# Kernel optimization log

Hardware: AMD Instinct MI355X
Metric: run time of the kernel (lower is better)

The kernel has to match this reference:

```python
import jax, jax.numpy as jnp
import numpy as np

B_SZ, L, D_INNER = 2, 1024, 2048
D_STATE, DT_RANK = 16, 64


def setup_inputs() -> dict:
    key = jax.random.key(0)
    k1, k2, k3, k4 = jax.random.split(key, 4)
    x = jax.random.normal(k1, (B_SZ, L, D_INNER), dtype=jnp.float32)
    # Linear weights: torch layout (out_features, in_features); scaled ~1/sqrt(fan_in)
    W_x = jax.random.normal(k2, (DT_RANK + 2 * D_STATE, D_INNER), dtype=jnp.float32) / np.sqrt(D_INNER)
    W_dt = jax.random.normal(k3, (D_INNER, DT_RANK), dtype=jnp.float32) / np.sqrt(DT_RANK)
    b_dt = jax.random.normal(k4, (D_INNER,), dtype=jnp.float32) * 0.1
    # A_log = log(arange(1, d_state+1)) broadcast to (d_inner, d_state), as in __init__
    A_log = jnp.broadcast_to(jnp.log(jnp.arange(1, D_STATE + 1, dtype=jnp.float32)), (D_INNER, D_STATE))
    D = jnp.ones((D_INNER,), dtype=jnp.float32)
    return {"x": x, "W_x": W_x, "W_dt": W_dt, "b_dt": b_dt, "A_log": A_log, "D": D}


def reference(x, W_x, W_dt, b_dt, A_log, D):
    # x: (B, L, d_inner)
    xz = jnp.einsum('bld,kd->blk', x, W_x)                       # (B, L, dt_rank + 2*d_state)
    delta_raw = xz[..., :DT_RANK]
    B_in = xz[..., DT_RANK:DT_RANK + D_STATE]                    # (B, L, d_state)
    C_in = xz[..., DT_RANK + D_STATE:]                           # (B, L, d_state)
    delta = jax.nn.softplus(jnp.einsum('blr,dr->bld', delta_raw, W_dt) + b_dt)  # (B, L, d_inner)
    A = -jnp.exp(A_log)                                          # (d_inner, d_state), negative
    A_bar = jnp.exp(delta[..., None] * A)                        # (B, L, d_inner, d_state)
    B_bar = delta[..., None] * B_in[:, :, None, :]               # (B, L, d_inner, d_state)

    def step(h, inputs):
        A_t, Bx_t, C_t = inputs                                  # (B,d,n), (B,d,n), (B,n)
        h = A_t * h + Bx_t
        y_t = jnp.sum(h * C_t[:, None, :], axis=-1)              # (B, d_inner)
        return h, y_t

    h0 = jnp.zeros((x.shape[0], D_INNER, D_STATE), dtype=x.dtype)
    Bx = B_bar * x[..., None]                                    # (B, L, d_inner, d_state)
    # scan over L: move L to leading axis
    _, ys = jax.lax.scan(step, h0, (jnp.moveaxis(A_bar, 1, 0), jnp.moveaxis(Bx, 1, 0), jnp.moveaxis(C_in, 1, 0)))
    y = jnp.moveaxis(ys, 0, 1) + D * x                           # (B, L, d_inner)
    return y
```

## Files before the change

### kernel.cpp

```cpp
#include <hip/hip_runtime.h>
#include <hip/hip_bf16.h>

#define B_SZ 2
#define LSEQ 1024
#define DIN  2048
#define DST  16
#define DTR  64
#define KTOT 96
#define NROW (B_SZ * LSEQ)
#define NCH  64
#define TCH  16
#define KSP  32

__device__ __forceinline__ float b2f(unsigned int u) {
    union { unsigned int i; float f; } v;
    v.i = (u & 0xffffu) << 16;
    return v.f;
}

__device__ __forceinline__ float ldf(const void* p, size_t i, bool f32) {
    return f32 ? ((const float*)p)[i] : b2f(((const unsigned short*)p)[i]);
}

__device__ __forceinline__ float4 ld4(const void* p, size_t i, bool f32) {
    if (f32) return *(const float4*)((const float*)p + i);
    const uint2 u = *(const uint2*)((const unsigned short*)p + i);
    float4 v;
    v.x = b2f(u.x); v.y = b2f(u.x >> 16);
    v.z = b2f(u.y); v.w = b2f(u.y >> 16);
    return v;
}

__device__ __forceinline__ float softplus_f(float v) {
    return (v > 20.f) ? v : log1pf(__expf(v));
}

__global__ __launch_bounds__(256) void k_detect(const void* __restrict__ x,
                                                int* __restrict__ flag) {
    __shared__ int cnt;
    if (threadIdx.x == 0) cnt = 0;
    __syncthreads();
    const unsigned short* u = (const unsigned short*)x;
    int my = 0;
    for (int i = threadIdx.x; i < 4096; i += 256) {
        unsigned short v = u[2 * i];
        float af = fabsf(b2f(v));
        if (v == 0 || (af >= 6.0e-8f && af <= 1.7e7f)) my++;
    }
    atomicAdd(&cnt, my);
    __syncthreads();
    if (threadIdx.x == 0) *flag = (cnt < 2048) ? 1 : 0;
}

__global__ __launch_bounds__(256, 4) void k_proj(
    const void* __restrict__ x,
    const void* __restrict__ Wx,
    const int*  __restrict__ flag,
    float* __restrict__ part)
{
    const bool f32 = (*flag != 0);
    __shared__ float lx[32][68];
    __shared__ float lw[32][100];
    const int tid = threadIdx.x;
    const int bx = blockIdx.x;
    const int by = blockIdx.y;
    const int rt = tid >> 4, ct = tid & 15;
    const int r0 = rt * 4, c0 = ct * 6;

    float acc[4][6];
    #pragma unroll
    for (int i = 0; i < 4; i++)
        #pragma unroll
        for (int k = 0; k < 6; k++) acc[i][k] = 0.f;

    for (int half = 0; half < 2; half++) {
        const int k0 = by * 64 + half * 32;
        #pragma unroll
        for (int it = 0; it < 2; it++) {
            const int idx = tid + it * 256;
            const int r = idx >> 3, q = idx & 7;
            float4 v = ld4(x, (size_t)(bx * 64 + r) * DIN + k0 + q * 4, f32);
            lx[q * 4 + 0][r] = v.x; lx[q * 4 + 1][r] = v.y;
            lx[q * 4 + 2][r] = v.z; lx[q * 4 + 3][r] = v.w;
        }
        #pragma unroll
        for (int it = 0; it < 3; it++) {
            const int idx = tid + it * 256;
            const int c = idx >> 3, q = idx & 7;
            float4 v = ld4(Wx, (size_t)c * DIN + k0 + q * 4, f32);
            lw[q * 4 + 0][c] = v.x; lw[q * 4 + 1][c] = v.y;
            lw[q * 4 + 2][c] = v.z; lw[q * 4 + 3][c] = v.w;
        }
        __syncthreads();

        #pragma unroll 4
        for (int j = 0; j < 32; j++) {
            const float4 xa = *(const float4*)&lx[j][r0];
            const float2 w0 = *(const float2*)&lw[j][c0];
            const float2 w1 = *(const float2*)&lw[j][c0 + 2];
            const float2 w2 = *(const float2*)&lw[j][c0 + 4];
            const float xr[4] = {xa.x, xa.y, xa.z, xa.w};
            const float wc[6] = {w0.x, w0.y, w1.x, w1.y, w2.x, w2.y};
            #pragma unroll
            for (int i = 0; i < 4; i++)
                #pragma unroll
                for (int k = 0; k < 6; k++)
                    acc[i][k] += xr[i] * wc[k];
        }
        __syncthreads();
    }

    float* p = part + ((size_t)by * NROW + bx * 64 + r0) * KTOT + c0;
    #pragma unroll
    for (int i = 0; i < 4; i++) {
        float* row = p + (size_t)i * KTOT;
        *(float2*)(row)     = make_float2(acc[i][0], acc[i][1]);
        *(float2*)(row + 2) = make_float2(acc[i][2], acc[i][3]);
        *(float2*)(row + 4) = make_float2(acc[i][4], acc[i][5]);
    }
}

__global__ __launch_bounds__(256, 4) void k_comb(
    const float* __restrict__ part,
    float* __restrict__ drw, float* __restrict__ Bin, float* __restrict__ Cin)
{
    const int idx = blockIdx.x * 256 + threadIdx.x;
    float s = 0.f;
    #pragma unroll 8
    for (int ks = 0; ks < KSP; ks++)
        s += part[(size_t)ks * NROW * KTOT + idx];
    const int r = idx / KTOT, c = idx % KTOT;
    if (c < DTR)            drw[r * DTR + c] = s;
    else if (c < DTR + DST) Bin[r * DST + (c - DTR)] = s;
    else                    Cin[r * DST + (c - DTR - DST)] = s;
}

__global__ __launch_bounds__(256, 4) void k_dt(
    const float* __restrict__ drw,
    const void* __restrict__ Wdt,
    const void* __restrict__ bdt,
    const int*  __restrict__ flag,
    float* __restrict__ dt)
{
    const bool f32 = (*flag != 0);
    __shared__ float la[64][68];
    __shared__ float lb[64][68];
    const int tid = threadIdx.x;
    const int r0g = blockIdx.x * 64, c0g = blockIdx.y * 64;

    #pragma unroll
    for (int it = 0; it < 4; it++) {
        const int idx = tid + it * 256;
        const int r = idx >> 4, q = idx & 15;
        float4 v = *(const float4*)(drw + (size_t)(r0g + r) * DTR + q * 4);
        la[q * 4 + 0][r] = v.x; la[q * 4 + 1][r] = v.y;
        la[q * 4 + 2][r] = v.z; la[q * 4 + 3][r] = v.w;
    }
    #pragma unroll
    for (int it = 0; it < 4; it++) {
        const int idx = tid + it * 256;
        const int c = idx >> 4, q = idx & 15;
        float4 v = ld4(Wdt, (size_t)(c0g + c) * DTR + q * 4, f32);
        lb[q * 4 + 0][c] = v.x; lb[q * 4 + 1][c] = v.y;
        lb[q * 4 + 2][c] = v.z; lb[q * 4 + 3][c] = v.w;
    }
    __syncthreads();

    const int rt = tid >> 4, ct = tid & 15;
    const int r0 = rt * 4, c0 = ct * 4;
    float acc[4][4];
    #pragma unroll
    for (int i = 0; i < 4; i++)
        #pragma unroll
        for (int k = 0; k < 4; k++) acc[i][k] = 0.f;

    #pragma unroll 8
    for (int j = 0; j < 64; j++) {
        const float4 a = *(const float4*)&la[j][r0];
        const float4 b = *(const float4*)&lb[j][c0];
        const float ar[4] = {a.x, a.y, a.z, a.w};
        const float bc[4] = {b.x, b.y, b.z, b.w};
        #pragma unroll
        for (int i = 0; i < 4; i++)
            #pragma unroll
            for (int k = 0; k < 4; k++)
                acc[i][k] += ar[i] * bc[k];
    }

    float bd[4];
    #pragma unroll
    for (int k = 0; k < 4; k++) bd[k] = ldf(bdt, (size_t)(c0g + c0 + k), f32);
    #pragma unroll
    for (int i = 0; i < 4; i++) {
        float4 o;
        o.x = softplus_f(acc[i][0] + bd[0]);
        o.y = softplus_f(acc[i][1] + bd[1]);
        o.z = softplus_f(acc[i][2] + bd[2]);
        o.w = softplus_f(acc[i][3] + bd[3]);
        *(float4*)(dt + (size_t)(r0g + r0 + i) * DIN + c0g + c0) = o;
    }
}

__global__ __launch_bounds__(256, 4) void k_scan1(
    const void* __restrict__ x,
    const float* __restrict__ dt,
    const float* __restrict__ Bin,
    const void* __restrict__ Alog,
    const int*  __restrict__ flag,
    float* __restrict__ Pb,
    float* __restrict__ Hb)
{
    const bool f32 = (*flag != 0);
    __shared__ float Bs[TCH * DST];
    const int tid = threadIdx.x;
    const int d = blockIdx.x * 256 + tid;
    const int c = blockIdx.y;
    const int b = blockIdx.z;
    const int row0 = b * LSEQ + c * TCH;

    if (tid < TCH * DST) Bs[tid] = Bin[(size_t)row0 * DST + tid];

    float A[DST];
    #pragma unroll
    for (int sq = 0; sq < DST / 4; sq++) {
        float4 av = ld4(Alog, (size_t)d * DST + sq * 4, f32);
        A[sq * 4 + 0] = -__expf(av.x); A[sq * 4 + 1] = -__expf(av.y);
        A[sq * 4 + 2] = -__expf(av.z); A[sq * 4 + 3] = -__expf(av.w);
    }
    __syncthreads();

    float P[DST], H[DST];
    #pragma unroll
    for (int s = 0; s < DST; s++) { P[s] = 1.f; H[s] = 0.f; }

    #pragma unroll 4
    for (int t = 0; t < TCH; t++) {
        const size_t off = (size_t)(row0 + t) * DIN + d;
        const float dtv = dt[off];
        const float xv  = ldf(x, off, f32);
        const float u   = dtv * xv;
        const float* bs = Bs + t * DST;
        #pragma unroll
        for (int s = 0; s < DST; s++) {
            const float e = __expf(dtv * A[s]);
            P[s] *= e;
            H[s] = e * H[s] + u * bs[s];
        }
    }

    const size_t base = (size_t)(b * NCH + c) * DST * DIN + d;
    #pragma unroll
    for (int s = 0; s < DST; s++) {
        Pb[base + (size_t)s * DIN] = P[s];
        Hb[base + (size_t)s * DIN] = H[s];
    }
}

__global__ __launch_bounds__(256, 4) void k_scan2(
    float* __restrict__ Pb,
    const float* __restrict__ Hb)
{
    const int idx = blockIdx.x * 256 + threadIdx.x;
    const int b   = idx / (DST * DIN);
    const int rem = idx % (DST * DIN);
    float h = 0.f;
    #pragma unroll 4
    for (int c = 0; c < NCH; c++) {
        const size_t o = (size_t)(b * NCH + c) * DST * DIN + rem;
        const float p = Pb[o], hb = Hb[o];
        Pb[o] = h;
        h = hb + p * h;
    }
}

__global__ __launch_bounds__(256, 4) void k_scan3(
    const void* __restrict__ x,
    const float* __restrict__ dt,
    const float* __restrict__ Bin,
    const float* __restrict__ Cin,
    const void* __restrict__ Alog,
    const void* __restrict__ Dv,
    const float* __restrict__ hin,
    const int*  __restrict__ flag,
    void* __restrict__ y)
{
    const bool f32 = (*flag != 0);
    __shared__ float Bs[TCH * DST];
    __shared__ float Cs[TCH * DST];
    const int tid = threadIdx.x;
    const int d = blockIdx.x * 256 + tid;
    const int c = blockIdx.y;
    const int b = blockIdx.z;
    const int row0 = b * LSEQ + c * TCH;

    if (tid < TCH * DST) {
        Bs[tid] = Bin[(size_t)row0 * DST + tid];
        Cs[tid] = Cin[(size_t)row0 * DST + tid];
    }

    float A[DST];
    #pragma unroll
    for (int sq = 0; sq < DST / 4; sq++) {
        float4 av = ld4(Alog, (size_t)d * DST + sq * 4, f32);
        A[sq * 4 + 0] = -__expf(av.x); A[sq * 4 + 1] = -__expf(av.y);
        A[sq * 4 + 2] = -__expf(av.z); A[sq * 4 + 3] = -__expf(av.w);
    }
    const float Dd = ldf(Dv, (size_t)d, f32);
    __syncthreads();

    float h[DST];
    const size_t base = (size_t)(b * NCH + c) * DST * DIN + d;
    #pragma unroll
    for (int s = 0; s < DST; s++) h[s] = hin[base + (size_t)s * DIN];

    #pragma unroll 4
    for (int t = 0; t < TCH; t++) {
        const size_t off = (size_t)(row0 + t) * DIN + d;
        const float dtv = dt[off];
        const float xv  = ldf(x, off, f32);
        const float u   = dtv * xv;
        const float* bs = Bs + t * DST;
        const float* cs = Cs + t * DST;
        float yv = Dd * xv;
        #pragma unroll
        for (int s = 0; s < DST; s++) {
            const float e = __expf(dtv * A[s]);
            h[s] = e * h[s] + u * bs[s];
            yv += h[s] * cs[s];
        }
        if (f32) ((float*)y)[off] = yv;
        else     ((__hip_bfloat16*)y)[off] = __float2bfloat16(yv);
    }
}

extern "C" void kernel_launch(void* const* d_in, const int* in_sizes, int n_in,
                              void* d_out, int out_size, void* d_ws, size_t ws_size,
                              hipStream_t stream) {
    const void* x    = d_in[0];
    const void* Wx   = d_in[1];
    const void* Wdt  = d_in[2];
    const void* bdt  = d_in[3];
    const void* Alog = d_in[4];
    const void* Dv   = d_in[5];

    int*   flag  = (int*)d_ws;
    float* basep = (float*)d_ws + 16;
    float* drw   = basep;
    float* Bin   = drw + (size_t)NROW * DTR;
    float* Cin   = Bin + (size_t)NROW * DST;
    float* part  = Cin + (size_t)NROW * DST;
    float* dt    = part + (size_t)KSP * NROW * KTOT;
    float* Pb    = dt + (size_t)NROW * DIN;
    float* Hb    = Pb + (size_t)B_SZ * NCH * DST * DIN;

    k_detect<<<1, 256, 0, stream>>>(x, flag);

    k_proj<<<dim3(NROW / 64, KSP), 256, 0, stream>>>(x, Wx, flag, part);

    k_comb<<<(NROW * KTOT) / 256, 256, 0, stream>>>(part, drw, Bin, Cin);

    k_dt<<<dim3(NROW / 64, DIN / 64), 256, 0, stream>>>(drw, Wdt, bdt, flag, dt);

    dim3 g1(DIN / 256, NCH, B_SZ);
    k_scan1<<<g1, 256, 0, stream>>>(x, dt, Bin, Alog, flag, Pb, Hb);

    k_scan2<<<(B_SZ * DST * DIN) / 256, 256, 0, stream>>>(Pb, Hb);

    k_scan3<<<g1, 256, 0, stream>>>(x, dt, Bin, Cin, Alog, Dv, Pb, flag, d_out);
}
```

Measured before the change: 173.0 us.

## Inline dtype detection into each kernel and halve scan chunk and split-K counts

Drops the separate single-block detect kernel. Each kernel now works out the input dtype itself from a smaller sample of x, which saves one launch and a serial dependency. Scan chunking changes from 64 chunks of 16 steps to 32 chunks of 32, and split-K goes from 32 to 16 slices. This shrinks the partial-sum and carry buffers at the cost of longer per-thread serial work and fewer blocks. The redundant per-block detection adds a few global reads and barriers to every block.

```diff
diff --git a/kernel.cpp b/kernel.cpp
--- a/kernel.cpp
+++ b/kernel.cpp
@@ -8,9 +8,9 @@
 #define DTR  64
 #define KTOT 96
 #define NROW (B_SZ * LSEQ)
-#define NCH  64
-#define TCH  16
-#define KSP  32
+#define NCH  32
+#define TCH  32
+#define KSP  16
 
 __device__ __forceinline__ float b2f(unsigned int u) {
     union { unsigned int i; float f; } v;
@@ -35,30 +35,28 @@
     return (v > 20.f) ? v : log1pf(__expf(v));
 }
 
-__global__ __launch_bounds__(256) void k_detect(const void* __restrict__ x,
-                                                int* __restrict__ flag) {
-    __shared__ int cnt;
-    if (threadIdx.x == 0) cnt = 0;
+__device__ __forceinline__ bool detect_f32(const void* x) {
+    __shared__ int det_cnt;
+    if (threadIdx.x == 0) det_cnt = 0;
     __syncthreads();
     const unsigned short* u = (const unsigned short*)x;
     int my = 0;
-    for (int i = threadIdx.x; i < 4096; i += 256) {
+    for (int i = threadIdx.x; i < 1024; i += 256) {
         unsigned short v = u[2 * i];
         float af = fabsf(b2f(v));
         if (v == 0 || (af >= 6.0e-8f && af <= 1.7e7f)) my++;
     }
-    atomicAdd(&cnt, my);
-    __syncthreads();
-    if (threadIdx.x == 0) *flag = (cnt < 2048) ? 1 : 0;
+    atomicAdd(&det_cnt, my);
+    __syncthreads();
+    return det_cnt < 512;
 }
 
 __global__ __launch_bounds__(256, 4) void k_proj(
     const void* __restrict__ x,
     const void* __restrict__ Wx,
-    const int*  __restrict__ flag,
     float* __restrict__ part)
 {
-    const bool f32 = (*flag != 0);
+    const bool f32 = detect_f32(x);
     __shared__ float lx[32][68];
     __shared__ float lw[32][100];
     const int tid = threadIdx.x;
@@ -73,8 +71,8 @@
         #pragma unroll
         for (int k = 0; k < 6; k++) acc[i][k] = 0.f;
 
-    for (int half = 0; half < 2; half++) {
-        const int k0 = by * 64 + half * 32;
+    for (int half = 0; half < 4; half++) {
+        const int k0 = by * 128 + half * 32;
         #pragma unroll
         for (int it = 0; it < 2; it++) {
             const int idx = tid + it * 256;
@@ -126,7 +124,7 @@
 {
     const int idx = blockIdx.x * 256 + threadIdx.x;
     float s = 0.f;
-    #pragma unroll 8
+    #pragma unroll
     for (int ks = 0; ks < KSP; ks++)
         s += part[(size_t)ks * NROW * KTOT + idx];
     const int r = idx / KTOT, c = idx % KTOT;
@@ -139,10 +137,10 @@
     const float* __restrict__ drw,
     const void* __restrict__ Wdt,
     const void* __restrict__ bdt,
-    const int*  __restrict__ flag,
+    const void* __restrict__ xdet,
     float* __restrict__ dt)
 {
-    const bool f32 = (*flag != 0);
+    const bool f32 = detect_f32(xdet);
     __shared__ float la[64][68];
     __shared__ float lb[64][68];
     const int tid = threadIdx.x;
@@ -206,11 +204,10 @@
     const float* __restrict__ dt,
     const float* __restrict__ Bin,
     const void* __restrict__ Alog,
-    const int*  __restrict__ flag,
     float* __restrict__ Pb,
     float* __restrict__ Hb)
 {
-    const bool f32 = (*flag != 0);
+    const bool f32 = detect_f32(x);
     __shared__ float Bs[TCH * DST];
     const int tid = threadIdx.x;
     const int d = blockIdx.x * 256 + tid;
@@ -218,7 +215,9 @@
     const int b = blockIdx.z;
     const int row0 = b * LSEQ + c * TCH;
 
-    if (tid < TCH * DST) Bs[tid] = Bin[(size_t)row0 * DST + tid];
+    #pragma unroll
+    for (int i = tid; i < TCH * DST; i += 256)
+        Bs[i] = Bin[(size_t)row0 * DST + i];
 
     float A[DST];
     #pragma unroll
@@ -281,10 +280,9 @@
     const void* __restrict__ Alog,
     const void* __restrict__ Dv,
     const float* __restrict__ hin,
-    const int*  __restrict__ flag,
     void* __restrict__ y)
 {
-    const bool f32 = (*flag != 0);
+    const bool f32 = detect_f32(x);
     __shared__ float Bs[TCH * DST];
     __shared__ float Cs[TCH * DST];
     const int tid = threadIdx.x;
@@ -293,9 +291,10 @@
     const int b = blockIdx.z;
     const int row0 = b * LSEQ + c * TCH;
 
-    if (tid < TCH * DST) {
-        Bs[tid] = Bin[(size_t)row0 * DST + tid];
-        Cs[tid] = Cin[(size_t)row0 * DST + tid];
+    #pragma unroll
+    for (int i = tid; i < TCH * DST; i += 256) {
+        Bs[i] = Bin[(size_t)row0 * DST + i];
+        Cs[i] = Cin[(size_t)row0 * DST + i];
     }
 
     float A[DST];
@@ -343,8 +342,7 @@
     const void* Alog = d_in[4];
     const void* Dv   = d_in[5];
 
-    int*   flag  = (int*)d_ws;
-    float* basep = (float*)d_ws + 16;
+    float* basep = (float*)d_ws;
     float* drw   = basep;
     float* Bin   = drw + (size_t)NROW * DTR;
     float* Cin   = Bin + (size_t)NROW * DST;
@@ -353,18 +351,16 @@
     float* Pb    = dt + (size_t)NROW * DIN;
     float* Hb    = Pb + (size_t)B_SZ * NCH * DST * DIN;
 
-    k_detect<<<1, 256, 0, stream>>>(x, flag);
-
-    k_proj<<<dim3(NROW / 64, KSP), 256, 0, stream>>>(x, Wx, flag, part);
+    k_proj<<<dim3(NROW / 64, KSP), 256, 0, stream>>>(x, Wx, part);
 
     k_comb<<<(NROW * KTOT) / 256, 256, 0, stream>>>(part, drw, Bin, Cin);
 
-    k_dt<<<dim3(NROW / 64, DIN / 64), 256, 0, stream>>>(drw, Wdt, bdt, flag, dt);
+    k_dt<<<dim3(NROW / 64, DIN / 64), 256, 0, stream>>>(drw, Wdt, bdt, x, dt);
 
     dim3 g1(DIN / 256, NCH, B_SZ);
-    k_scan1<<<g1, 256, 0, stream>>>(x, dt, Bin, Alog, flag, Pb, Hb);
+    k_scan1<<<g1, 256, 0, stream>>>(x, dt, Bin, Alog, Pb, Hb);
 
     k_scan2<<<(B_SZ * DST * DIN) / 256, 256, 0, stream>>>(Pb, Hb);
 
-    k_scan3<<<g1, 256, 0, stream>>>(x, dt, Bin, Cin, Alog, Dv, Pb, flag, d_out);
-}
+    k_scan3<<<g1, 256, 0, stream>>>(x, dt, Bin, Cin, Alog, Dv, Pb, d_out);
+}
```

Result: slower. 180.7 us (+4.5%).
